# Performance work log

Hardware: AMD Instinct MI355X
Metric: run time of the kernel (lower is better)

Reference implementation:

```python
import jax, jax.numpy as jnp
import numpy as np

B = 8192
I_SIZE = 1024
H_SIZE = 1024
C2 = 2.7183  # module's hard-coded e approximation

def setup_inputs() -> dict:
    key = jax.random.key(0)
    k0, k1, k2, k3, k4 = jax.random.split(key, 5)
    input_tensor = jax.random.uniform(k0, (B, I_SIZE + 1), dtype=jnp.float32)  # last col = dt >= 0
    h_cur = jax.random.normal(k1, (B, H_SIZE), dtype=jnp.float32)
    c_cur = jax.random.normal(k2, (B, H_SIZE), dtype=jnp.float32)
    W_layers = jax.random.normal(k3, (4 * H_SIZE, I_SIZE + H_SIZE), dtype=jnp.float32) * 0.02
    b_layers = jnp.zeros((4 * H_SIZE,), dtype=jnp.float32)
    W_desc = jax.random.normal(k4, (H_SIZE, H_SIZE), dtype=jnp.float32) * 0.02
    b_desc = jnp.zeros((H_SIZE,), dtype=jnp.float32)
    return {"input_tensor": input_tensor, "h_cur": h_cur, "c_cur": c_cur,
            "W_layers": W_layers, "b_layers": b_layers,
            "W_desc": W_desc, "b_desc": b_desc}

def reference(input_tensor, h_cur, c_cur, W_layers, b_layers, W_desc, b_desc):
    x = input_tensor[:, :-1]          # [B, I]
    dt = input_tensor[:, -1:]         # [B, 1]
    # map_elapse_time: T = 1/log(t + e), broadcast over h_size (matmul with ones == broadcast)
    T = 1.0 / jnp.log(dt + C2)        # [B, 1]
    C_ST = jnp.tanh(h_cur @ W_desc.T + b_desc)          # [B, H]
    h_adj = h_cur - C_ST + T * C_ST                     # decayed short-term memory
    combined = jnp.concatenate([x, h_adj], axis=1)      # [B, I+H]
    gates = combined @ W_layers.T + b_layers            # [B, 4H]
    cc_i, cc_f, cc_o, cc_g = jnp.split(gates, 4, axis=1)
    i = jax.nn.sigmoid(cc_i)
    f = jax.nn.sigmoid(cc_f)
    o = jax.nn.sigmoid(cc_o)
    g = jnp.tanh(cc_g)
    c_next = f * c_cur + i * g
    h_next = o * jnp.tanh(c_next)
    return (h_next, c_next)
```

## Files before the change

### kernel.cpp

```cpp
#include <hip/hip_runtime.h>
#include <hip/hip_bf16.h>
#include <math.h>

typedef __bf16 bf16x8 __attribute__((ext_vector_type(8)));
typedef float  f32x4  __attribute__((ext_vector_type(4)));

#define B_ROWS 8192
#define HSZ    1024

#define GLOAD16(gsrc, ldst)                                                          \
  __builtin_amdgcn_global_load_lds((const __attribute__((address_space(1))) void*)(gsrc), \
                                   (__attribute__((address_space(3))) void*)(ldst),  \
                                   16, 0, 0)

__device__ inline unsigned short f2bf(float f) {
  union { float f; unsigned u; } x; x.f = f;
  unsigned r = x.u + 0x7fffu + ((x.u >> 16) & 1u);
  return (unsigned short)(r >> 16);
}

__device__ inline void store4bf(unsigned short* p, float4 v) {
  ushort4 u;
  u.x = f2bf(v.x); u.y = f2bf(v.y); u.z = f2bf(v.z); u.w = f2bf(v.w);
  *(ushort4*)p = u;
}

__device__ inline float sigm(float x) { return 1.0f / (1.0f + __expf(-x)); }

__global__ void k_convert(const float* __restrict__ inp,
                          const float* __restrict__ h,
                          const float* __restrict__ Wl,
                          const float* __restrict__ Wd,
                          unsigned short* __restrict__ comb,
                          unsigned short* __restrict__ Wlb,
                          unsigned short* __restrict__ hb,
                          unsigned short* __restrict__ Wdb,
                          float* __restrict__ Tm1) {
  const long stride = (long)gridDim.x * blockDim.x;
  const long tid0 = (long)blockIdx.x * blockDim.x + threadIdx.x;

  for (long i = tid0; i < (long)B_ROWS * HSZ / 4; i += stride) {
    float4 v = ((const float4*)h)[i];
    store4bf(hb + i * 4, v);
  }
  for (long i = tid0; i < (long)B_ROWS * HSZ / 4; i += stride) {
    long e = i * 4; long b = e >> 10; long c = e & 1023;
    float4 v = *(const float4*)(inp + b * 1025 + c);
    store4bf(comb + b * 2048 + c, v);
  }
  for (long i = tid0; i < 4096L * 2048 / 4; i += stride) {
    float4 v = ((const float4*)Wl)[i];
    store4bf(Wlb + i * 4, v);
  }
  for (long i = tid0; i < 1024L * 1024 / 4; i += stride) {
    float4 v = ((const float4*)Wd)[i];
    store4bf(Wdb + i * 4, v);
  }
  for (long i = tid0; i < B_ROWS; i += stride) {
    float dt = inp[i * 1025 + 1024];
    Tm1[i] = 1.0f / logf(dt + 2.7183f) - 1.0f;
  }
}

__global__ void k_gemm1(const unsigned short* __restrict__ A,
                        const unsigned short* __restrict__ Bm,
                        const float* __restrict__ h,
                        const float* __restrict__ bd,
                        const float* __restrict__ Tm1,
                        unsigned short* __restrict__ comb) {
  const int K = 1024;
  __shared__ __align__(16) unsigned short As[128 * 32];
  __shared__ __align__(16) unsigned short Bs[128 * 32];
  const int tid = threadIdx.x;
  const int lane = tid & 63;
  const int wave = tid >> 6;
  const int wr = wave >> 1, wc = wave & 1;
  const int bRow = blockIdx.x;
  const int bCol = blockIdx.y;

  const int sRow = tid >> 2;
  const int sK = (tid & 3) * 8;
  const unsigned short* aSrc0 = A + (long)(bRow * 128 + sRow) * K + sK;
  const unsigned short* aSrc1 = A + (long)(bRow * 128 + 64 + sRow) * K + sK;
  const unsigned short* bSrc0 = Bm + (long)(bCol * 128 + sRow) * K + sK;
  const unsigned short* bSrc1 = Bm + (long)(bCol * 128 + 64 + sRow) * K + sK;
  unsigned short* aDst0 = As + tid * 8;
  unsigned short* aDst1 = As + 2048 + tid * 8;
  unsigned short* bDst0 = Bs + tid * 8;
  unsigned short* bDst1 = Bs + 2048 + tid * 8;

  f32x4 acc[4][4] = {};
  const int fr = lane & 15, fk = (lane >> 4) * 8;

  for (int k0 = 0; k0 < K; k0 += 32) {
    GLOAD16(aSrc0 + k0, aDst0);
    GLOAD16(aSrc1 + k0, aDst1);
    GLOAD16(bSrc0 + k0, bDst0);
    GLOAD16(bSrc1 + k0, bDst1);
    __syncthreads();
    bf16x8 a[4], b[4];
#pragma unroll
    for (int m = 0; m < 4; m++) a[m] = *(const bf16x8*)(As + (wr * 64 + m * 16 + fr) * 32 + fk);
#pragma unroll
    for (int n = 0; n < 4; n++) b[n] = *(const bf16x8*)(Bs + (wc * 64 + n * 16 + fr) * 32 + fk);
#pragma unroll
    for (int m = 0; m < 4; m++)
#pragma unroll
      for (int n = 0; n < 4; n++)
        acc[m][n] = __builtin_amdgcn_mfma_f32_16x16x32_bf16(a[m], b[n], acc[m][n], 0, 0, 0);
    __syncthreads();
  }

  const int cr = (lane >> 4) * 4;
  const int cc = lane & 15;
#pragma unroll
  for (int m = 0; m < 4; m++)
#pragma unroll
    for (int n = 0; n < 4; n++) {
      const int col = bCol * 128 + wc * 64 + n * 16 + cc;
#pragma unroll
      for (int r = 0; r < 4; r++) {
        const int row = bRow * 128 + wr * 64 + m * 16 + cr + r;
        float v = acc[m][n][r] + bd[col];
        float cst = tanhf(v);
        float hadj = h[(long)row * HSZ + col] + Tm1[row] * cst;
        comb[(long)row * 2048 + 1024 + col] = f2bf(hadj);
      }
    }
}

__global__ void k_gemm2(const unsigned short* __restrict__ A,
                        const unsigned short* __restrict__ Bm,
                        const float* __restrict__ bl,
                        const float* __restrict__ c_cur,
                        float* __restrict__ out) {
  const int K = 2048;
  __shared__ __align__(16) unsigned short As[128 * 32];
  __shared__ __align__(16) unsigned short Bs[128 * 32];
  const int tid = threadIdx.x;
  const int lane = tid & 63;
  const int wave = tid >> 6;
  const int wr = wave >> 1, wc = wave & 1;
  const int bRow = blockIdx.x;
  const int bj = blockIdx.y;

  const int sRow = tid >> 2;
  const int sK = (tid & 3) * 8;
  const int rl0 = sRow, rl1 = 64 + sRow;
  const unsigned short* aSrc0 = A + (long)(bRow * 128 + sRow) * K + sK;
  const unsigned short* aSrc1 = A + (long)(bRow * 128 + 64 + sRow) * K + sK;
  const unsigned short* bSrc0 = Bm + (long)((rl0 >> 5) * 1024 + bj * 32 + (rl0 & 31)) * K + sK;
  const unsigned short* bSrc1 = Bm + (long)((rl1 >> 5) * 1024 + bj * 32 + (rl1 & 31)) * K + sK;
  unsigned short* aDst0 = As + tid * 8;
  unsigned short* aDst1 = As + 2048 + tid * 8;
  unsigned short* bDst0 = Bs + tid * 8;
  unsigned short* bDst1 = Bs + 2048 + tid * 8;

  f32x4 acc[4][4] = {};
  const int fr = lane & 15, fk = (lane >> 4) * 8;

  for (int k0 = 0; k0 < K; k0 += 32) {
    GLOAD16(aSrc0 + k0, aDst0);
    GLOAD16(aSrc1 + k0, aDst1);
    GLOAD16(bSrc0 + k0, bDst0);
    GLOAD16(bSrc1 + k0, bDst1);
    __syncthreads();
    bf16x8 a[4], b[4];
#pragma unroll
    for (int m = 0; m < 4; m++) a[m] = *(const bf16x8*)(As + (wr * 64 + m * 16 + fr) * 32 + fk);
#pragma unroll
    for (int n = 0; n < 4; n++) b[n] = *(const bf16x8*)(Bs + (n * 32 + wc * 16 + fr) * 32 + fk);
#pragma unroll
    for (int m = 0; m < 4; m++)
#pragma unroll
      for (int n = 0; n < 4; n++)
        acc[m][n] = __builtin_amdgcn_mfma_f32_16x16x32_bf16(a[m], b[n], acc[m][n], 0, 0, 0);
    __syncthreads();
  }

  const int cr = (lane >> 4) * 4;
  const int cc = lane & 15;
  const int j = bj * 32 + wc * 16 + cc;
#pragma unroll
  for (int m = 0; m < 4; m++) {
#pragma unroll
    for (int r = 0; r < 4; r++) {
      const int row = bRow * 128 + wr * 64 + m * 16 + cr + r;
      float iv = sigm(acc[m][0][r] + bl[j]);
      float fv = sigm(acc[m][1][r] + bl[1024 + j]);
      float ov = sigm(acc[m][2][r] + bl[2048 + j]);
      float gv = tanhf(acc[m][3][r] + bl[3072 + j]);
      float cn = fv * c_cur[(long)row * HSZ + j] + iv * gv;
      float hn = ov * tanhf(cn);
      out[(long)row * HSZ + j] = hn;
      out[(long)B_ROWS * HSZ + (long)row * HSZ + j] = cn;
    }
  }
}

extern "C" void kernel_launch(void* const* d_in, const int* in_sizes, int n_in,
                              void* d_out, int out_size, void* d_ws, size_t ws_size,
                              hipStream_t stream) {
  const float* inp = (const float*)d_in[0];
  const float* h   = (const float*)d_in[1];
  const float* c   = (const float*)d_in[2];
  const float* Wl  = (const float*)d_in[3];
  const float* bl  = (const float*)d_in[4];
  const float* Wd  = (const float*)d_in[5];
  const float* bd  = (const float*)d_in[6];

  char* ws = (char*)d_ws;
  unsigned short* comb = (unsigned short*)(ws);
  unsigned short* Wlb  = (unsigned short*)(ws + 33554432);
  unsigned short* hb   = (unsigned short*)(ws + 50331648);
  unsigned short* Wdb  = (unsigned short*)(ws + 67108864);
  float*          Tm1  = (float*)(ws + 69206016);
  float*          out  = (float*)d_out;

  hipLaunchKernelGGL(k_convert, dim3(2048), dim3(256), 0, stream,
                     inp, h, Wl, Wd, comb, Wlb, hb, Wdb, Tm1);
  hipLaunchKernelGGL(k_gemm1, dim3(64, 8), dim3(256), 0, stream,
                     hb, Wdb, h, bd, Tm1, comb);
  hipLaunchKernelGGL(k_gemm2, dim3(64, 32), dim3(256), 0, stream,
                     comb, Wlb, bl, c, out);
}
```

Before: 259.4 us.

## Rewrite gate GEMM with 256x256 tiles, 4-stage LDS pipeline and swizzle

Replaces the gate GEMM with a 512-thread kernel that computes 256x256 output tiles. Operand tiles stream through a 4-buffer LDS ring with global_load_lds prefetch three steps ahead, and the MFMA work is split into two phases with priority boosts. LDS rows use an XOR swizzle to avoid bank conflicts, and block indices are remapped for L2 locality. The aim is to raise arithmetic intensity and hide global latency, at the cost of higher register and LDS use (128KB LDS per block) and fragile manual waitcnt and barrier logic.

```diff
diff --git a/kernel.cpp b/kernel.cpp
--- a/kernel.cpp
+++ b/kernel.cpp
@@ -129,63 +129,112 @@
     }
 }
 
-__global__ void k_gemm2(const unsigned short* __restrict__ A,
-                        const unsigned short* __restrict__ Bm,
-                        const float* __restrict__ bl,
-                        const float* __restrict__ c_cur,
-                        float* __restrict__ out) {
-  const int K = 2048;
-  __shared__ __align__(16) unsigned short As[128 * 32];
-  __shared__ __align__(16) unsigned short Bs[128 * 32];
+#define NT2 64
+__global__ __launch_bounds__(512, 2)
+void k_gemm2_8ph(const unsigned short* __restrict__ A,
+                 const unsigned short* __restrict__ Bm,
+                 const float* __restrict__ bl,
+                 const float* __restrict__ c_cur,
+                 float* __restrict__ out) {
+  __shared__ __align__(16) unsigned short lds[4][16384];
+
   const int tid = threadIdx.x;
   const int lane = tid & 63;
-  const int wave = tid >> 6;
-  const int wr = wave >> 1, wc = wave & 1;
-  const int bRow = blockIdx.x;
-  const int bj = blockIdx.y;
-
-  const int sRow = tid >> 2;
-  const int sK = (tid & 3) * 8;
-  const int rl0 = sRow, rl1 = 64 + sRow;
-  const unsigned short* aSrc0 = A + (long)(bRow * 128 + sRow) * K + sK;
-  const unsigned short* aSrc1 = A + (long)(bRow * 128 + 64 + sRow) * K + sK;
-  const unsigned short* bSrc0 = Bm + (long)((rl0 >> 5) * 1024 + bj * 32 + (rl0 & 31)) * K + sK;
-  const unsigned short* bSrc1 = Bm + (long)((rl1 >> 5) * 1024 + bj * 32 + (rl1 & 31)) * K + sK;
-  unsigned short* aDst0 = As + tid * 8;
-  unsigned short* aDst1 = As + 2048 + tid * 8;
-  unsigned short* bDst0 = Bs + tid * 8;
-  unsigned short* bDst1 = Bs + 2048 + tid * 8;
-
-  f32x4 acc[4][4] = {};
-  const int fr = lane & 15, fk = (lane >> 4) * 8;
-
-  for (int k0 = 0; k0 < K; k0 += 32) {
-    GLOAD16(aSrc0 + k0, aDst0);
-    GLOAD16(aSrc1 + k0, aDst1);
-    GLOAD16(bSrc0 + k0, bDst0);
-    GLOAD16(bSrc1 + k0, bDst1);
-    __syncthreads();
+  const int wid = tid >> 6;
+  const int wr = wid >> 2;
+  const int wc = wid & 3;
+
+  const int bid = blockIdx.x;
+  const int swz = (bid & 7) * 64 + (bid >> 3);
+  const int bRow = swz & 31;
+  const int bCol = swz >> 5;
+
+  const int sr = tid >> 2;
+  const int swsel = (sr >> 1) & 3;
+  const int gk = ((tid & 3) ^ swsel) << 3;
+  const unsigned short* aBase = A + (long)(bRow * 256 + sr) * 2048 + gk;
+  const int rl0 = sr, rl1 = 128 + sr;
+  const int grow0 = ((rl0 >> 4) & 3) * 1024 + bCol * 64 + (rl0 >> 6) * 16 + (rl0 & 15);
+  const int grow1 = ((rl1 >> 4) & 3) * 1024 + bCol * 64 + (rl1 >> 6) * 16 + (rl1 & 15);
+  const unsigned short* bBase0 = Bm + (long)grow0 * 2048 + gk;
+  const unsigned short* bBase1 = Bm + (long)grow1 * 2048 + gk;
+
+#define STAGE_A2(tt) { unsigned short* d_ = &lds[(tt) & 3][0] + tid * 8;          \
+    GLOAD16(aBase + (long)(tt) * 32, d_);                                          \
+    GLOAD16(aBase + 128L * 2048 + (long)(tt) * 32, d_ + 512 * 8); }
+#define STAGE_B2(tt) { unsigned short* d_ = &lds[(tt) & 3][8192] + tid * 8;       \
+    GLOAD16(bBase0 + (long)(tt) * 32, d_);                                         \
+    GLOAD16(bBase1 + (long)(tt) * 32, d_ + 512 * 8); }
+
+  const int fr = lane & 15, q = lane >> 4;
+  int offA[8], offB[4];
+#pragma unroll
+  for (int m = 0; m < 8; m++) {
+    const int row = wr * 128 + m * 16 + fr;
+    offA[m] = row * 32 + ((q ^ ((row >> 1) & 3)) << 3);
+  }
+#pragma unroll
+  for (int n = 0; n < 4; n++) {
+    const int row = wc * 64 + n * 16 + fr;
+    offB[n] = 8192 + row * 32 + ((q ^ ((row >> 1) & 3)) << 3);
+  }
+
+  f32x4 acc[8][4] = {};
+
+  STAGE_A2(0); STAGE_B2(0);
+  STAGE_A2(1); STAGE_B2(1);
+  STAGE_A2(2); STAGE_B2(2);
+  asm volatile("s_waitcnt vmcnt(8)" ::: "memory");
+  __builtin_amdgcn_sched_barrier(0);
+  __builtin_amdgcn_s_barrier();
+
+  for (int t = 0; t < NT2; ++t) {
+    const unsigned short* buf = lds[t & 3];
     bf16x8 a[4], b[4];
 #pragma unroll
-    for (int m = 0; m < 4; m++) a[m] = *(const bf16x8*)(As + (wr * 64 + m * 16 + fr) * 32 + fk);
-#pragma unroll
-    for (int n = 0; n < 4; n++) b[n] = *(const bf16x8*)(Bs + (n * 32 + wc * 16 + fr) * 32 + fk);
+    for (int m = 0; m < 4; m++) a[m] = *(const bf16x8*)(buf + offA[m]);
+#pragma unroll
+    for (int n = 0; n < 4; n++) b[n] = *(const bf16x8*)(buf + offB[n]);
+    if (t < NT2 - 3) STAGE_A2(t + 3);
+    __builtin_amdgcn_s_barrier();
+    asm volatile("s_waitcnt lgkmcnt(0)" ::: "memory");
+    __builtin_amdgcn_sched_barrier(0);
+    __builtin_amdgcn_s_setprio(1);
 #pragma unroll
     for (int m = 0; m < 4; m++)
 #pragma unroll
       for (int n = 0; n < 4; n++)
         acc[m][n] = __builtin_amdgcn_mfma_f32_16x16x32_bf16(a[m], b[n], acc[m][n], 0, 0, 0);
-    __syncthreads();
+    __builtin_amdgcn_s_setprio(0);
+    __builtin_amdgcn_s_barrier();
+#pragma unroll
+    for (int m = 0; m < 4; m++) a[m] = *(const bf16x8*)(buf + offA[m + 4]);
+    if (t < NT2 - 3) STAGE_B2(t + 3);
+    __builtin_amdgcn_s_barrier();
+    asm volatile("s_waitcnt lgkmcnt(0)" ::: "memory");
+    __builtin_amdgcn_sched_barrier(0);
+    __builtin_amdgcn_s_setprio(1);
+#pragma unroll
+    for (int m = 0; m < 4; m++)
+#pragma unroll
+      for (int n = 0; n < 4; n++)
+        acc[m + 4][n] = __builtin_amdgcn_mfma_f32_16x16x32_bf16(a[m], b[n], acc[m + 4][n], 0, 0, 0);
+    __builtin_amdgcn_s_setprio(0);
+    if (t < NT2 - 3)       { asm volatile("s_waitcnt vmcnt(8)" ::: "memory"); }
+    else if (t == NT2 - 3) { asm volatile("s_waitcnt vmcnt(4)" ::: "memory"); }
+    else if (t == NT2 - 2) { asm volatile("s_waitcnt vmcnt(0)" ::: "memory"); }
+    __builtin_amdgcn_sched_barrier(0);
+    __builtin_amdgcn_s_barrier();
   }
 
   const int cr = (lane >> 4) * 4;
   const int cc = lane & 15;
-  const int j = bj * 32 + wc * 16 + cc;
-#pragma unroll
-  for (int m = 0; m < 4; m++) {
+  const int j = bCol * 64 + wc * 16 + cc;
+#pragma unroll
+  for (int m = 0; m < 8; m++) {
 #pragma unroll
     for (int r = 0; r < 4; r++) {
-      const int row = bRow * 128 + wr * 64 + m * 16 + cr + r;
+      const int row = bRow * 256 + wr * 128 + m * 16 + cr + r;
       float iv = sigm(acc[m][0][r] + bl[j]);
       float fv = sigm(acc[m][1][r] + bl[1024 + j]);
       float ov = sigm(acc[m][2][r] + bl[2048 + j]);
@@ -221,6 +270,6 @@
                      inp, h, Wl, Wd, comb, Wlb, hb, Wdb, Tm1);
   hipLaunchKernelGGL(k_gemm1, dim3(64, 8), dim3(256), 0, stream,
                      hb, Wdb, h, bd, Tm1, comb);
-  hipLaunchKernelGGL(k_gemm2, dim3(64, 32), dim3(256), 0, stream,
+  hipLaunchKernelGGL(k_gemm2_8ph, dim3(512), dim3(512), 0, stream,
                      comb, Wlb, bl, c, out);
 }
```

Result: faster. 243.0 us (-6.3%).

## Rewrite gate GEMM with 256x256 tiles, double-buffered LDS and XCD-aware block mapping

Applied to the files above, without the earlier changes.

The gate GEMM is replaced by a 512-thread kernel that computes 256x256 output tiles (64 columns of each of the four gates) with K-step 64. LDS is double-buffered and uses an XOR swizzle, and staging of the next tile is interleaved with MFMA quarters under explicit vmcnt/lgkmcnt waits and barriers. Blocks are remapped so each XCD works on a contiguous band of rows, which should improve L2 reuse. The aim is to cut global-load latency stalls and redundant operand traffic in the dominant GEMM. The cost is higher register and LDS pressure (128 KB of LDS, 2 blocks per CU) and fragile hand-written synchronisation.

```diff
diff --git a/kernel.cpp b/kernel.cpp
--- a/kernel.cpp
+++ b/kernel.cpp
@@ -129,63 +129,113 @@
     }
 }
 
-__global__ void k_gemm2(const unsigned short* __restrict__ A,
-                        const unsigned short* __restrict__ Bm,
-                        const float* __restrict__ bl,
-                        const float* __restrict__ c_cur,
-                        float* __restrict__ out) {
-  const int K = 2048;
-  __shared__ __align__(16) unsigned short As[128 * 32];
-  __shared__ __align__(16) unsigned short Bs[128 * 32];
+#define NKT 32
+#define BAR() __builtin_amdgcn_s_barrier()
+#define LGKM0() { asm volatile("s_waitcnt lgkmcnt(0)" ::: "memory"); __builtin_amdgcn_sched_barrier(0); }
+#define VMW(n) { asm volatile("s_waitcnt vmcnt(" #n ")" ::: "memory"); __builtin_amdgcn_sched_barrier(0); }
+
+__global__ __launch_bounds__(512, 2)
+void k_gemm2_q(const unsigned short* __restrict__ A,
+               const unsigned short* __restrict__ Bm,
+               const float* __restrict__ bl,
+               const float* __restrict__ c_cur,
+               float* __restrict__ out) {
+  __shared__ __align__(16) unsigned short lds2[2][32768];
+
   const int tid = threadIdx.x;
   const int lane = tid & 63;
-  const int wave = tid >> 6;
-  const int wr = wave >> 1, wc = wave & 1;
-  const int bRow = blockIdx.x;
-  const int bj = blockIdx.y;
-
-  const int sRow = tid >> 2;
-  const int sK = (tid & 3) * 8;
-  const int rl0 = sRow, rl1 = 64 + sRow;
-  const unsigned short* aSrc0 = A + (long)(bRow * 128 + sRow) * K + sK;
-  const unsigned short* aSrc1 = A + (long)(bRow * 128 + 64 + sRow) * K + sK;
-  const unsigned short* bSrc0 = Bm + (long)((rl0 >> 5) * 1024 + bj * 32 + (rl0 & 31)) * K + sK;
-  const unsigned short* bSrc1 = Bm + (long)((rl1 >> 5) * 1024 + bj * 32 + (rl1 & 31)) * K + sK;
-  unsigned short* aDst0 = As + tid * 8;
-  unsigned short* aDst1 = As + 2048 + tid * 8;
-  unsigned short* bDst0 = Bs + tid * 8;
-  unsigned short* bDst1 = Bs + 2048 + tid * 8;
-
-  f32x4 acc[4][4] = {};
-  const int fr = lane & 15, fk = (lane >> 4) * 8;
-
-  for (int k0 = 0; k0 < K; k0 += 32) {
-    GLOAD16(aSrc0 + k0, aDst0);
-    GLOAD16(aSrc1 + k0, aDst1);
-    GLOAD16(bSrc0 + k0, bDst0);
-    GLOAD16(bSrc1 + k0, bDst1);
-    __syncthreads();
-    bf16x8 a[4], b[4];
-#pragma unroll
-    for (int m = 0; m < 4; m++) a[m] = *(const bf16x8*)(As + (wr * 64 + m * 16 + fr) * 32 + fk);
-#pragma unroll
-    for (int n = 0; n < 4; n++) b[n] = *(const bf16x8*)(Bs + (n * 32 + wc * 16 + fr) * 32 + fk);
-#pragma unroll
-    for (int m = 0; m < 4; m++)
-#pragma unroll
-      for (int n = 0; n < 4; n++)
-        acc[m][n] = __builtin_amdgcn_mfma_f32_16x16x32_bf16(a[m], b[n], acc[m][n], 0, 0, 0);
-    __syncthreads();
+  const int wid = tid >> 6;
+  const int wr = wid >> 2;
+  const int wc = wid & 3;
+
+  const int bid = blockIdx.x;
+  const int xcd = bid & 7;
+  const int ii = bid >> 3;
+  const int sweep = ii >> 5;
+  const int pos = ii & 31;
+  const int bRow = xcd * 4 + sweep * 2 + (pos & 1);
+  const int bCol = pos >> 1;
+
+  const int strow = tid >> 3;
+  const int gkswz = ((tid & 7) ^ (strow & 7)) << 3;
+  const unsigned short* aS[4]; const unsigned short* bS[4];
+#pragma unroll
+  for (int q4 = 0; q4 < 4; q4++) {
+    aS[q4] = A  + (long)(bRow * 256 + q4 * 64 + strow) * 2048 + gkswz;
+    bS[q4] = Bm + (long)(q4 * 1024 + bCol * 64 + strow) * 2048 + gkswz;
+  }
+#define STG_AH(dd, kt, hh) { \
+    GLOAD16(aS[(hh)*2 + 0] + (kt)*64, &lds2[dd][(hh)*8192 + 0    + tid*8]); \
+    GLOAD16(aS[(hh)*2 + 1] + (kt)*64, &lds2[dd][(hh)*8192 + 4096 + tid*8]); }
+#define STG_BH(dd, kt, hh) { \
+    GLOAD16(bS[(hh)*2 + 0] + (kt)*64, &lds2[dd][16384 + (hh)*8192 + 0    + tid*8]); \
+    GLOAD16(bS[(hh)*2 + 1] + (kt)*64, &lds2[dd][16384 + (hh)*8192 + 4096 + tid*8]); }
+
+  const int fr = lane & 15, q = lane >> 4;
+  const int c80 = ((q)     ^ (fr & 7)) << 3;
+  const int c81 = ((4 + q) ^ (fr & 7)) << 3;
+  const int aoff0 = wr * 8192 + fr * 64 + c80;
+  const int aoff1 = wr * 8192 + fr * 64 + c81;
+  const int boff0 = 16384 + (wc * 16 + fr) * 64 + c80;
+  const int boff1 = 16384 + (wc * 16 + fr) * 64 + c81;
+
+#define RD_A(dd, mq) { _Pragma("unroll") for (int m = 0; m < 4; m++) { \
+    aFk0[m] = *(const bf16x8*)(&lds2[dd][aoff0 + (mq)*4096 + m*1024]); \
+    aFk1[m] = *(const bf16x8*)(&lds2[dd][aoff1 + (mq)*4096 + m*1024]); } }
+#define RD_B(dd, nq, b_k0, b_k1) { _Pragma("unroll") for (int n2 = 0; n2 < 2; n2++) { \
+    b_k0[n2] = *(const bf16x8*)(&lds2[dd][boff0 + (nq)*8192 + n2*4096]); \
+    b_k1[n2] = *(const bf16x8*)(&lds2[dd][boff1 + (nq)*8192 + n2*4096]); } }
+#define MF(mq, nq, b_k0, b_k1) { \
+  __builtin_amdgcn_s_setprio(1); \
+  _Pragma("unroll") for (int m = 0; m < 4; m++) \
+    _Pragma("unroll") for (int n2 = 0; n2 < 2; n2++) \
+      acc[(mq)*4+m][(nq)*2+n2] = __builtin_amdgcn_mfma_f32_16x16x32_bf16(aFk0[m], b_k0[n2], acc[(mq)*4+m][(nq)*2+n2], 0, 0, 0); \
+  _Pragma("unroll") for (int m = 0; m < 4; m++) \
+    _Pragma("unroll") for (int n2 = 0; n2 < 2; n2++) \
+      acc[(mq)*4+m][(nq)*2+n2] = __builtin_amdgcn_mfma_f32_16x16x32_bf16(aFk1[m], b_k1[n2], acc[(mq)*4+m][(nq)*2+n2], 0, 0, 0); \
+  __builtin_amdgcn_s_setprio(0); \
+  __builtin_amdgcn_sched_barrier(0); }
+
+  f32x4 acc[8][4] = {};
+  bf16x8 aFk0[4], aFk1[4], b0k0[2], b0k1[2], b1k0[2], b1k1[2];
+
+  STG_AH(0, 0, 0); STG_AH(0, 0, 1); STG_BH(0, 0, 0); STG_BH(0, 0, 1);
+  VMW(2); BAR();
+
+  for (int t = 0; t < NKT; ++t) {
+    const int d = t & 1, dn = d ^ 1;
+    const bool more = (t < NKT - 1);
+    RD_A(d, 0); RD_B(d, 0, b0k0, b0k1);
+    if (more) STG_AH(dn, t + 1, 0);
+    BAR(); LGKM0();
+    MF(0, 0, b0k0, b0k1);
+    if (more) { VMW(2); } else { VMW(0); }
+    BAR();
+    RD_B(d, 1, b1k0, b1k1);
+    if (more) STG_AH(dn, t + 1, 1);
+    BAR(); LGKM0();
+    MF(0, 1, b1k0, b1k1);
+    BAR();
+    RD_A(d, 1);
+    if (more) STG_BH(dn, t + 1, 0);
+    BAR(); LGKM0();
+    MF(1, 1, b1k0, b1k1);
+    BAR();
+    if (more) STG_BH(dn, t + 1, 1);
+    BAR();
+    MF(1, 0, b0k0, b0k1);
+    VMW(2);
+    BAR();
   }
 
   const int cr = (lane >> 4) * 4;
   const int cc = lane & 15;
-  const int j = bj * 32 + wc * 16 + cc;
-#pragma unroll
-  for (int m = 0; m < 4; m++) {
+  const int j = bCol * 64 + wc * 16 + cc;
+#pragma unroll
+  for (int m = 0; m < 8; m++) {
 #pragma unroll
     for (int r = 0; r < 4; r++) {
-      const int row = bRow * 128 + wr * 64 + m * 16 + cr + r;
+      const int row = bRow * 256 + wr * 128 + m * 16 + cr + r;
       float iv = sigm(acc[m][0][r] + bl[j]);
       float fv = sigm(acc[m][1][r] + bl[1024 + j]);
       float ov = sigm(acc[m][2][r] + bl[2048 + j]);
@@ -221,6 +271,6 @@
                      inp, h, Wl, Wd, comb, Wlb, hb, Wdb, Tm1);
   hipLaunchKernelGGL(k_gemm1, dim3(64, 8), dim3(256), 0, stream,
                      hb, Wdb, h, bd, Tm1, comb);
-  hipLaunchKernelGGL(k_gemm2, dim3(64, 32), dim3(256), 0, stream,
+  hipLaunchKernelGGL(k_gemm2_q, dim3(512), dim3(512), 0, stream,
                      comb, Wlb, bl, c, out);
 }
```

Result: faster. 227.0 us (-12.5%).

## Rewrite gate GEMM with 256x256 tiles, triple-buffered LDS A and register-streamed B

Applied to the files above, without the earlier changes.

The second GEMM now uses 512-thread blocks computing 256 rows by 64 columns of each of the four gates, with K-tiles of 64. A is staged into a triple-buffered, XOR-swizzled LDS ring. B fragments are loaded straight from global memory into double-buffered registers. Blocks are remapped so that column tiles are grouped per XCD for L2 reuse, and s_setprio plus explicit waitcnt/barrier scheduling is used to overlap loads with MFMA. The aim is more reuse per tile and less LDS traffic and sync overhead, at the cost of higher register pressure from the 8x4 accumulators and the B prefetch.

```diff
diff --git a/kernel.cpp b/kernel.cpp
--- a/kernel.cpp
+++ b/kernel.cpp
@@ -129,63 +129,114 @@
     }
 }
 
-__global__ void k_gemm2(const unsigned short* __restrict__ A,
-                        const unsigned short* __restrict__ Bm,
-                        const float* __restrict__ bl,
-                        const float* __restrict__ c_cur,
-                        float* __restrict__ out) {
-  const int K = 2048;
-  __shared__ __align__(16) unsigned short As[128 * 32];
-  __shared__ __align__(16) unsigned short Bs[128 * 32];
+#define NKT3 32
+__global__ __launch_bounds__(512, 2)
+void k_gemm2_bd(const unsigned short* __restrict__ A,
+                const unsigned short* __restrict__ Bm,
+                const float* __restrict__ bl,
+                const float* __restrict__ c_cur,
+                float* __restrict__ out) {
+  __shared__ __align__(16) unsigned short ldsA[3][16384];
+
   const int tid = threadIdx.x;
   const int lane = tid & 63;
-  const int wave = tid >> 6;
-  const int wr = wave >> 1, wc = wave & 1;
-  const int bRow = blockIdx.x;
-  const int bj = blockIdx.y;
-
-  const int sRow = tid >> 2;
-  const int sK = (tid & 3) * 8;
-  const int rl0 = sRow, rl1 = 64 + sRow;
-  const unsigned short* aSrc0 = A + (long)(bRow * 128 + sRow) * K + sK;
-  const unsigned short* aSrc1 = A + (long)(bRow * 128 + 64 + sRow) * K + sK;
-  const unsigned short* bSrc0 = Bm + (long)((rl0 >> 5) * 1024 + bj * 32 + (rl0 & 31)) * K + sK;
-  const unsigned short* bSrc1 = Bm + (long)((rl1 >> 5) * 1024 + bj * 32 + (rl1 & 31)) * K + sK;
-  unsigned short* aDst0 = As + tid * 8;
-  unsigned short* aDst1 = As + 2048 + tid * 8;
-  unsigned short* bDst0 = Bs + tid * 8;
-  unsigned short* bDst1 = Bs + 2048 + tid * 8;
-
-  f32x4 acc[4][4] = {};
-  const int fr = lane & 15, fk = (lane >> 4) * 8;
-
-  for (int k0 = 0; k0 < K; k0 += 32) {
-    GLOAD16(aSrc0 + k0, aDst0);
-    GLOAD16(aSrc1 + k0, aDst1);
-    GLOAD16(bSrc0 + k0, bDst0);
-    GLOAD16(bSrc1 + k0, bDst1);
-    __syncthreads();
-    bf16x8 a[4], b[4];
-#pragma unroll
-    for (int m = 0; m < 4; m++) a[m] = *(const bf16x8*)(As + (wr * 64 + m * 16 + fr) * 32 + fk);
-#pragma unroll
-    for (int n = 0; n < 4; n++) b[n] = *(const bf16x8*)(Bs + (n * 32 + wc * 16 + fr) * 32 + fk);
-#pragma unroll
-    for (int m = 0; m < 4; m++)
-#pragma unroll
-      for (int n = 0; n < 4; n++)
-        acc[m][n] = __builtin_amdgcn_mfma_f32_16x16x32_bf16(a[m], b[n], acc[m][n], 0, 0, 0);
-    __syncthreads();
-  }
+  const int wid = tid >> 6;
+  const int wr = wid >> 2;
+  const int wc = wid & 3;
+
+  const int bid = blockIdx.x;
+  const int xcd = bid & 7;
+  const int ii = bid >> 3;
+  const int bCol = xcd * 2 + (ii & 1);
+  const int bRow = ii >> 1;
+
+  const int strow = tid >> 3;
+  const int gkswz = ((tid & 7) ^ (strow & 7)) << 3;
+  const unsigned short* aS0 = A + (long)(bRow * 256 +   0 + strow) * 2048 + gkswz;
+  const unsigned short* aS1 = A + (long)(bRow * 256 +  64 + strow) * 2048 + gkswz;
+  const unsigned short* aS2 = A + (long)(bRow * 256 + 128 + strow) * 2048 + gkswz;
+  const unsigned short* aS3 = A + (long)(bRow * 256 + 192 + strow) * 2048 + gkswz;
+#define STG_A(bb, kt) {                                   \
+    GLOAD16(aS0 + (long)(kt) * 64, &ldsA[bb][    0 + tid * 8]); \
+    GLOAD16(aS1 + (long)(kt) * 64, &ldsA[bb][ 4096 + tid * 8]); \
+    GLOAD16(aS2 + (long)(kt) * 64, &ldsA[bb][ 8192 + tid * 8]); \
+    GLOAD16(aS3 + (long)(kt) * 64, &ldsA[bb][12288 + tid * 8]); }
+
+  const int fr = lane & 15, q = lane >> 4;
+  const unsigned short* bD0 = Bm + (long)(           bCol * 64 + wc * 16 + fr) * 2048 + q * 8;
+  const unsigned short* bD1 = Bm + (long)(1024 +     bCol * 64 + wc * 16 + fr) * 2048 + q * 8;
+  const unsigned short* bD2 = Bm + (long)(2048 +     bCol * 64 + wc * 16 + fr) * 2048 + q * 8;
+  const unsigned short* bD3 = Bm + (long)(3072 +     bCol * 64 + wc * 16 + fr) * 2048 + q * 8;
+#define LOADB(dst, kt) {                                         \
+    dst[0][0] = *(const bf16x8*)(bD0 + (long)(kt) * 64);         \
+    dst[0][1] = *(const bf16x8*)(bD0 + (long)(kt) * 64 + 32);    \
+    dst[1][0] = *(const bf16x8*)(bD1 + (long)(kt) * 64);         \
+    dst[1][1] = *(const bf16x8*)(bD1 + (long)(kt) * 64 + 32);    \
+    dst[2][0] = *(const bf16x8*)(bD2 + (long)(kt) * 64);         \
+    dst[2][1] = *(const bf16x8*)(bD2 + (long)(kt) * 64 + 32);    \
+    dst[3][0] = *(const bf16x8*)(bD3 + (long)(kt) * 64);         \
+    dst[3][1] = *(const bf16x8*)(bD3 + (long)(kt) * 64 + 32); }
+
+  int aoff0[8], aoff1[8];
+#pragma unroll
+  for (int m = 0; m < 8; m++) {
+    const int row = wr * 128 + m * 16 + fr;
+    const int base = (row >> 6) * 4096 + (row & 63) * 64;
+    aoff0[m] = base + (((q)     ^ (fr & 7)) << 3);
+    aoff1[m] = base + (((4 + q) ^ (fr & 7)) << 3);
+  }
+
+  f32x4 acc[8][4] = {};
+  bf16x8 bPA[4][2], bPB[4][2];
+
+  LOADB(bPA, 0);
+  STG_A(0, 0);
+  STG_A(1, 1);
+
+#define TILE3(t, cur, nxt) {                                                        \
+    asm volatile("s_waitcnt lgkmcnt(0)" ::: "memory");                              \
+    if ((t) < NKT3 - 1) { asm volatile("s_waitcnt vmcnt(4)" ::: "memory"); }        \
+    else                { asm volatile("s_waitcnt vmcnt(0)" ::: "memory"); }        \
+    __builtin_amdgcn_sched_barrier(0);                                              \
+    __builtin_amdgcn_s_barrier();                                                   \
+    __builtin_amdgcn_sched_barrier(0);                                              \
+    if ((t) + 1 < NKT3) LOADB(nxt, (t) + 1);                                        \
+    if ((t) + 2 < NKT3) STG_A(((t) + 2) % 3, (t) + 2);                              \
+    const unsigned short* buf = ldsA[(t) % 3];                                      \
+    __builtin_amdgcn_s_setprio(1);                                                  \
+    _Pragma("unroll")                                                               \
+    for (int mq = 0; mq < 2; mq++) {                                                \
+      bf16x8 aF0[4], aF1[4];                                                        \
+      _Pragma("unroll")                                                             \
+      for (int m = 0; m < 4; m++) {                                                 \
+        aF0[m] = *(const bf16x8*)(buf + aoff0[mq * 4 + m]);                         \
+        aF1[m] = *(const bf16x8*)(buf + aoff1[mq * 4 + m]);                         \
+      }                                                                             \
+      _Pragma("unroll")                                                             \
+      for (int m = 0; m < 4; m++)                                                   \
+        _Pragma("unroll")                                                           \
+        for (int g = 0; g < 4; g++) {                                               \
+          acc[mq * 4 + m][g] = __builtin_amdgcn_mfma_f32_16x16x32_bf16(aF0[m], cur[g][0], acc[mq * 4 + m][g], 0, 0, 0); \
+          acc[mq * 4 + m][g] = __builtin_amdgcn_mfma_f32_16x16x32_bf16(aF1[m], cur[g][1], acc[mq * 4 + m][g], 0, 0, 0); \
+        }                                                                           \
+    }                                                                               \
+    __builtin_amdgcn_s_setprio(0);                                                  \
+  }
+
+  for (int t = 0; t < NKT3; t += 2) {
+    TILE3(t,     bPA, bPB);
+    TILE3(t + 1, bPB, bPA);
+  }
+#undef TILE3
 
   const int cr = (lane >> 4) * 4;
   const int cc = lane & 15;
-  const int j = bj * 32 + wc * 16 + cc;
-#pragma unroll
-  for (int m = 0; m < 4; m++) {
+  const int j = bCol * 64 + wc * 16 + cc;
+#pragma unroll
+  for (int m = 0; m < 8; m++) {
 #pragma unroll
     for (int r = 0; r < 4; r++) {
-      const int row = bRow * 128 + wr * 64 + m * 16 + cr + r;
+      const int row = bRow * 256 + wr * 128 + m * 16 + cr + r;
       float iv = sigm(acc[m][0][r] + bl[j]);
       float fv = sigm(acc[m][1][r] + bl[1024 + j]);
       float ov = sigm(acc[m][2][r] + bl[2048 + j]);
@@ -221,6 +272,6 @@
                      inp, h, Wl, Wd, comb, Wlb, hb, Wdb, Tm1);
   hipLaunchKernelGGL(k_gemm1, dim3(64, 8), dim3(256), 0, stream,
                      hb, Wdb, h, bd, Tm1, comb);
-  hipLaunchKernelGGL(k_gemm2, dim3(64, 32), dim3(256), 0, stream,
+  hipLaunchKernelGGL(k_gemm2_bd, dim3(512), dim3(512), 0, stream,
                      comb, Wlb, bl, c, out);
 }
```

Result: slower. 282.4 us (+8.9%).
